# Optimization experiments

Measured on AMD Instinct MI355X. Metric: run time of the kernel, lower is better.

## Reference

```python
import jax, jax.numpy as jnp
import numpy as np

B, S, L = 32, 50, 16            # batch, seq_len, lectures per step
C, D = 50, 64                   # num_concepts, hidden_dim (key=value=summary dim)
NQ, NL, NU = 10000, 2000, 5000  # num_items, num_nonassessed_items, num_users
QV = NQ + NL + 1                # q_embed vocab (questions + lectures + pad)
QAV = 2 * NQ + 1                # qa_embed vocab
H4 = 4 * D                      # linear_dim = 4 * value_dim
EPS = 1e-5                      # torch LayerNorm default eps


def setup_inputs() -> dict:
    ks = jax.random.split(jax.random.key(0), 16)
    rn = lambda k, sh, sc: jax.random.normal(k, sh, jnp.float32) * sc
    return dict(
        q_data=jax.random.randint(ks[0], (B, S), 0, QV),
        qa_data=jax.random.randint(ks[1], (B, S), 0, QAV),
        l_data=jax.random.randint(ks[2], (B, S, L), 0, QV),
        users=jax.random.randint(ks[3], (B,), 0, NU + 1),
        key_matrix=rn(ks[4], (C, D), (2.0 / D) ** 0.5),   # key_matrix_embed rows 1..C (kaiming)
        q_embed=rn(ks[5], (QV, D), 0.02),
        qa_embed=rn(ks[6], (QAV, D), 0.02),
        u_embed=rn(ks[7], (NU + 1, D), 0.02),             # looked up but unused by write()
        M0=rn(ks[8], (C, D), (2.0 / D) ** 0.5),           # kaiming-init value matrix
        W_e=rn(ks[9], (D, D), D ** -0.5), b_e=jnp.zeros((D,), jnp.float32),
        W_a=rn(ks[10], (D, D), D ** -0.5), b_a=jnp.zeros((D,), jnp.float32),
        ln_gamma=jnp.ones((H4,), jnp.float32), ln_beta=jnp.zeros((H4,), jnp.float32),
        W0=rn(ks[11], (H4, H4), H4 ** -0.5), b0=jnp.zeros((H4,), jnp.float32),
        W1=rn(ks[12], (H4, H4), H4 ** -0.5), b1=jnp.zeros((H4,), jnp.float32),
        W_out=rn(ks[13], (H4, 1), H4 ** -0.5), b_out=jnp.zeros((1,), jnp.float32),
    )


def _forward(q_data, qa_data, l_data, key_matrix, q_embed, qa_embed, M0,
             W_e, b_e, W_a, b_a, ln_gamma, ln_beta, W0, b0, W1, b1, W_out, b_out):
    Bv = q_data.shape[0]
    q_e = q_embed[q_data]        # (B,S,D)
    qa_e = qa_embed[qa_data]     # (B,S,D)
    l_e = q_embed[l_data]        # (B,S,L,D) lectures share the q embedding table

    corr = lambda x: jax.nn.softmax(x @ key_matrix.T, axis=-1)  # softmax addressing
    q_cw = corr(q_e)             # (B,S,C)
    l_cw = corr(l_e)             # (B,S,L,C)
    # erase / add gates are memory-independent -> precompute (batched GEMMs)
    l_er = jax.nn.sigmoid(l_e @ W_e + b_e); l_ad = jnp.tanh(l_e @ W_a + b_a)
    q_er = jax.nn.sigmoid(qa_e @ W_e + b_e); q_ad = jnp.tanh(qa_e @ W_a + b_a)

    tm2 = lambda x: jnp.swapaxes(x, 0, 1)           # (B,S,..) -> (S,B,..)
    tm3 = lambda x: jnp.transpose(x, (1, 2, 0, 3))  # (B,S,L,..) -> (S,L,B,..)
    xs = (tm2(q_cw), tm2(q_e), tm2(q_er), tm2(q_ad),
          tm3(l_cw), tm3(l_e), tm3(l_er), tm3(l_ad))

    def write(M, w, e, a):  # erase-add gated write
        w = w[:, :, None]   # (B,C,1)
        return M * (1.0 - w * e[:, None, :]) + w * a[:, None, :]

    def layer_norm(x):
        mu = jnp.mean(x, -1, keepdims=True)
        v = jnp.var(x, -1, keepdims=True)
        return (x - mu) * jax.lax.rsqrt(v + EPS) * ln_gamma + ln_beta

    def outer(M, step):
        qcw, q, qer, qad, lcw, le, ler, lad = step
        q_read = jnp.einsum('bc,bcd->bd', qcw, M)  # read BEFORE lecture writes

        def inner(carry, lx):
            Mc, acc = carry
            w, e, a = lx
            acc = acc + jnp.einsum('bc,bcd->bd', w, Mc)  # read then write
            return (write(Mc, w, e, a), acc), None

        (M, l_read), _ = jax.lax.scan(inner, (M, jnp.zeros_like(q)), (lcw, ler, lad))
        # `l` after the loop is the LAST lecture embedding of this step
        mastery = layer_norm(jnp.concatenate([q_read, q, l_read, le[-1]], axis=-1))
        h = jax.nn.relu(mastery @ W0 + b0) @ W1 + b1   # dropout = identity (eval)
        pred = jax.nn.sigmoid(h @ W_out + b_out)[:, 0]
        M = write(M, qcw, qer, qad)                    # commit the q/a interaction
        return M, pred

    M_init = jnp.broadcast_to(M0, (Bv,) + M0.shape)
    _, preds = jax.lax.scan(outer, M_init, xs)
    return jnp.swapaxes(preds, 0, 1)                   # (B,S)


def reference(q_data, qa_data, l_data, users, key_matrix, q_embed, qa_embed,
              u_embed, M0, W_e, b_e, W_a, b_a, ln_gamma, ln_beta,
              W0, b0, W1, b1, W_out, b_out):
    # users/u_embed are looked up by the torch module but unused by write()'s math
    return _forward(q_data, qa_data, l_data, key_matrix, q_embed, qa_embed, M0,
                    W_e, b_e, W_a, b_a, ln_gamma, ln_beta, W0, b0, W1, b1, W_out, b_out)
```

## Files before the change

### kernel.cpp

```cpp
#include <hip/hip_runtime.h>
#include <math.h>

#define BB 32
#define SS 50
#define LL 16
#define CC 50
#define DD 64
#define NCH 13
#define H4 256
#define NROWS_Q (BB*SS)
#define NROWS_L (BB*SS*LL)

#define EA_ST 2304
#define W_ST  68

#define RB 64
#define NBLK_L (NROWS_L/RB)
#define NBLK_Q (NROWS_Q/RB)
#define NGB (NBLK_L + 2*NBLK_Q)

#define KBAT 16
#define NBAT (H4/KBAT)

static_assert(EA_ST == 17*128 + 128, "ea record: 17 slots x 64 lanes x float2, +pad");
static_assert(W_ST == 17*4, "w record: 17 slots x 4 chunk-cols");
static_assert(SS % 2 == 0, "phaseA double-step pipeline needs even SS");
static_assert(NROWS_L % RB == 0 && NROWS_Q % RB == 0, "GEMM row blocking");
static_assert(NBAT*KBAT == H4 && NBAT % 2 == 0,
              "phaseB k-loop must cover ALL of H4 in pairs of batches");

#define OFF_EA     ((size_t)0)
#define OFF_W      (OFF_EA + (size_t)NROWS_Q*EA_ST)
#define OFF_PQ     (OFF_W  + (size_t)BB*NCH*SS*W_ST)
#define OFF_PL     (OFF_PQ + (size_t)NROWS_Q*DD)
#define OFF_QE     (OFF_PL + (size_t)NROWS_Q*DD)
#define OFF_LELAST (OFF_QE + (size_t)NROWS_Q*DD)

__global__ __launch_bounds__(256) void k0_kernel(
    const int* __restrict__ qd, const int* __restrict__ qadx,
    const int* __restrict__ ld,
    const float* __restrict__ Kmat, const float* __restrict__ qemb,
    const float* __restrict__ qaemb,
    const float* __restrict__ We, const float* __restrict__ Wa,
    const float* __restrict__ be, const float* __restrict__ ba,
    float* __restrict__ eaW, float* __restrict__ wrecW,
    float* __restrict__ Pzero,
    float* __restrict__ q_e_o, float* __restrict__ le_last)
{
    __shared__ float smem[16384];
    float* sX   = smem;
    float* sW   = smem + 4096;
    float* sOut = smem + 4096;

    int tid = threadIdx.x;
    int bid = blockIdx.x;

    for (int i = bid*256 + tid; i < 2*NROWS_Q*DD; i += NGB*256) Pzero[i] = 0.f;

    int bt, base;
    if (bid < NBLK_L)              { bt = 0; base = bid*RB; }
    else if (bid < NBLK_L+NBLK_Q)  { bt = 1; base = (bid-NBLK_L)*RB; }
    else                           { bt = 2; base = (bid-NBLK_L-NBLK_Q)*RB; }

    {
        const int*   idsrc = (bt==0) ? ld : (bt==1) ? qd : qadx;
        const float* tab   = (bt==2) ? qaemb : qemb;
        for (int idx = tid; idx < RB*16; idx += 256) {
            int r = idx >> 4, q = idx & 15;
            int id = idsrc[base + r];
            *(float4*)(sX + r*64 + q*4) =
                *(const float4*)(tab + (size_t)id*DD + q*4);
        }
    }
    for (int i = tid; i < 12288; i += 256) {
        int k4 = i / 768, rem = i - k4*768;
        int c = rem >> 2, j = rem & 3;
        int k = k4*4 + j;
        float v;
        if      (c < 64)  v = We[k*64 + c];
        else if (c < 128) v = Wa[k*64 + (c-64)];
        else if (c < 178) v = Kmat[(c-128)*64 + k];
        else              v = 0.f;
        sW[i] = v;
    }
    __syncthreads();

    int rg = tid >> 5, cg = tid & 31;
    int r0 = rg*8, c0 = cg*6;
    float acc[8][6];
    #pragma unroll
    for (int i = 0; i < 8; ++i)
        #pragma unroll
        for (int c = 0; c < 6; ++c) acc[i][c] = 0.f;

    #pragma unroll 2
    for (int k4 = 0; k4 < 16; ++k4) {
        float4 xv[8], wv[6];
        #pragma unroll
        for (int i = 0; i < 8; ++i)
            xv[i] = *(const float4*)(sX + (r0+i)*64 + k4*4);
        #pragma unroll
        for (int c = 0; c < 6; ++c)
            wv[c] = *(const float4*)(sW + k4*768 + (c0+c)*4);
        #pragma unroll
        for (int i = 0; i < 8; ++i)
            #pragma unroll
            for (int c = 0; c < 6; ++c) {
                acc[i][c] = fmaf(xv[i].x, wv[c].x, acc[i][c]);
                acc[i][c] = fmaf(xv[i].y, wv[c].y, acc[i][c]);
                acc[i][c] = fmaf(xv[i].z, wv[c].z, acc[i][c]);
                acc[i][c] = fmaf(xv[i].w, wv[c].w, acc[i][c]);
            }
    }
    __syncthreads();
    #pragma unroll
    for (int i = 0; i < 8; ++i)
        #pragma unroll
        for (int c = 0; c < 6; ++c)
            sOut[(r0+i)*192 + c0 + c] = acc[i][c];
    __syncthreads();

    int lane = tid & 63, wvi = tid >> 6;
    float bev = be[lane], bav = ba[lane];

    auto rowsoftmax = [&](const float* orow) -> float {
        float sc = orow[128 + lane];
        float s = (lane < CC) ? sc : -1e30f;
        float mx = s;
        #pragma unroll
        for (int o = 32; o >= 1; o >>= 1) mx = fmaxf(mx, __shfl_xor(mx, o));
        float p = (lane < CC) ? expf(s - mx) : 0.f;
        float sum = p;
        #pragma unroll
        for (int o = 32; o >= 1; o >>= 1) sum += __shfl_xor(sum, o);
        return p / sum;
    };

    for (int i = 0; i < 16; ++i) {
        int rr = wvi*16 + i;
        int grow = base + rr;
        const float* orow = sOut + rr*192;

        if (bt == 0) {
            float erv = 1.f / (1.f + expf(-(orow[lane] + bev)));
            float adv = tanhf(orow[64 + lane] + bav);
            float wsm = rowsoftmax(orow);
            int bs = grow >> 4, il = grow & 15;
            *(float2*)(eaW + (size_t)bs*EA_ST + il*128 + lane*2) =
                make_float2(erv, adv);
            int b = bs / SS, s2 = bs - b*SS;
            if (lane < 52) {
                int omx = lane >> 2, j = lane & 3;
                wrecW[(((size_t)(b*NCH + omx)*SS + s2)*17 + il)*4 + j] =
                    (lane < CC) ? wsm : 0.f;
            }
            if (il == LL-1) le_last[(size_t)bs*DD + lane] = sX[rr*64 + lane];
        } else if (bt == 1) {
            float wsm = rowsoftmax(orow);
            int qrow = grow;
            int b = qrow / SS, s2 = qrow - b*SS;
            if (lane < 52) {
                int omx = lane >> 2, j = lane & 3;
                wrecW[(((size_t)(b*NCH + omx)*SS + s2)*17 + 16)*4 + j] =
                    (lane < CC) ? wsm : 0.f;
            }
            q_e_o[(size_t)qrow*DD + lane] = sX[rr*64 + lane];
        } else {
            float erv = 1.f / (1.f + expf(-(orow[lane] + bev)));
            float adv = tanhf(orow[64 + lane] + bav);
            int qrow = grow;
            *(float2*)(eaW + (size_t)qrow*EA_ST + 2048 + lane*2) =
                make_float2(erv, adv);
        }
    }
}

__global__ __launch_bounds__(64) void phaseA_kernel(
    const float* __restrict__ M0,
    const float* __restrict__ ea, const float* __restrict__ wrec,
    float* __restrict__ Pq, float* __restrict__ Pl)
{
    int om   = blockIdx.x >> 5;
    int b    = blockIdx.x & 31;
    int lane = threadIdx.x;
    int c0   = om * 4;

    __shared__ __align__(16) float wbuf[2][W_ST];

    float M[4];
    #pragma unroll
    for (int i = 0; i < 4; ++i) {
        int c = c0 + i;
        M[i] = (c < CC) ? M0[c*DD + lane] : 0.f;
    }

    const float* eb = ea   + (size_t)b*SS*EA_ST + lane*2;
    const float* wb = wrec + (size_t)(b*NCH + om)*SS*W_ST;
    float* pq = Pq + (size_t)b*SS*DD + lane;
    float* pl = Pl + (size_t)b*SS*DD + lane;

    float2 ea0[17], ea1[17];

    #pragma unroll
    for (int il = 0; il < 17; ++il)
        ea0[il] = *(const float2*)(eb + il*128);
    if (lane < 17)
        *(float4*)&wbuf[0][lane*4] = *(const float4*)(wb + lane*4);

    auto step = [&](int s, float2 (&cur)[17], float2 (&nxt)[17], int wbsel) {
        bool pf = (s < SS-1);
        float4 rw;
        if (pf) {
            const float* eg = eb + (size_t)(s+1)*EA_ST;
            #pragma unroll
            for (int il = 0; il < 17; ++il)
                nxt[il] = *(const float2*)(eg + il*128);
            if (lane < 17)
                rw = *(const float4*)(wb + (size_t)(s+1)*W_ST + lane*4);
        }

        float4 qw = *(const float4*)&wbuf[wbsel][64];
        float qr;
        qr = qw.x * M[0];
        qr = fmaf(qw.y, M[1], qr);
        qr = fmaf(qw.z, M[2], qr);
        qr = fmaf(qw.w, M[3], qr);

        float a0 = 0.f, a1 = 0.f, a2 = 0.f, a3 = 0.f;
        #pragma unroll
        for (int il = 0; il < 16; ++il) {
            float4 w = *(const float4*)&wbuf[wbsel][il*4];
            float e = cur[il].x, a = cur[il].y;
            a0 = fmaf(w.x, M[0], a0);
            a1 = fmaf(w.y, M[1], a1);
            a2 = fmaf(w.z, M[2], a2);
            a3 = fmaf(w.w, M[3], a3);
            M[0] = fmaf(w.x, fmaf(-e, M[0], a), M[0]);
            M[1] = fmaf(w.y, fmaf(-e, M[1], a), M[1]);
            M[2] = fmaf(w.z, fmaf(-e, M[2], a), M[2]);
            M[3] = fmaf(w.w, fmaf(-e, M[3], a), M[3]);
        }

        atomicAdd(pq + (size_t)s*DD, qr);
        atomicAdd(pl + (size_t)s*DD, (a0 + a1) + (a2 + a3));

        {
            float e = cur[16].x, a = cur[16].y;
            M[0] = fmaf(qw.x, fmaf(-e, M[0], a), M[0]);
            M[1] = fmaf(qw.y, fmaf(-e, M[1], a), M[1]);
            M[2] = fmaf(qw.z, fmaf(-e, M[2], a), M[2]);
            M[3] = fmaf(qw.w, fmaf(-e, M[3], a), M[3]);
        }

        if (pf && lane < 17)
            *(float4*)&wbuf[wbsel ^ 1][lane*4] = rw;
    };

    for (int s = 0; s < SS; s += 2) {
        step(s,     ea0, ea1, 0);
        step(s + 1, ea1, ea0, 1);
    }
}

__global__ __launch_bounds__(256) void phaseB_kernel(
    const float* __restrict__ Pq, const float* __restrict__ Pl,
    const float* __restrict__ q_e_i, const float* __restrict__ le_last,
    const float* __restrict__ ln_g, const float* __restrict__ ln_b,
    const float* __restrict__ W0, const float* __restrict__ b0,
    const float* __restrict__ W1, const float* __restrict__ b1,
    const float* __restrict__ Wout, const float* __restrict__ bout,
    float* __restrict__ out)
{
    __shared__ float m[8][H4];
    __shared__ float h[8][H4];
    __shared__ float red[8][4];

    int j = threadIdx.x;
    int g0 = blockIdx.x * 8;
    int lane = j & 63, wv = j >> 6;

    int seg = j >> 6, dd = j & 63;
    #pragma unroll
    for (int r = 0; r < 8; ++r) {
        int g = g0 + r;
        float v;
        if      (seg == 0) v = Pq[(size_t)g*DD + dd];
        else if (seg == 1) v = q_e_i[(size_t)g*DD + dd];
        else if (seg == 2) v = Pl[(size_t)g*DD + dd];
        else               v = le_last[(size_t)g*DD + dd];
        m[r][j] = v;
    }
    __syncthreads();

    #pragma unroll
    for (int rr = 0; rr < 2; ++rr) {
        int r = wv + rr*4;
        float4 v4 = *(((const float4*)&m[r][0]) + lane);
        float s1 = v4.x + v4.y + v4.z + v4.w;
        float s2 = v4.x*v4.x + v4.y*v4.y + v4.z*v4.z + v4.w*v4.w;
        #pragma unroll
        for (int o = 32; o >= 1; o >>= 1) {
            s1 += __shfl_xor(s1, o);
            s2 += __shfl_xor(s2, o);
        }
        float mu  = s1 * (1.f/256.f);
        float var = s2 * (1.f/256.f) - mu*mu;
        float is  = rsqrtf(var + 1e-5f);
        float4 g4 = *(((const float4*)ln_g) + lane);
        float4 b4 = *(((const float4*)ln_b) + lane);
        float4 o4;
        o4.x = (v4.x - mu)*is*g4.x + b4.x;
        o4.y = (v4.y - mu)*is*g4.y + b4.y;
        o4.z = (v4.z - mu)*is*g4.z + b4.z;
        o4.w = (v4.w - mu)*is*g4.w + b4.w;
        *(((float4*)&m[r][0]) + lane) = o4;
    }
    __syncthreads();

    const float* Wp = W0 + j;
    float acc[8];
    {
        float bj = b0[j];
        #pragma unroll
        for (int r = 0; r < 8; ++r) acc[r] = bj;
    }
    {
        float wA[KBAT], wB[KBAT];
        #pragma unroll
        for (int t = 0; t < KBAT; ++t) wA[t] = Wp[(size_t)t*H4];
        #pragma unroll 1
        for (int kb = 0; kb < NBAT; kb += 2) {
            #pragma unroll
            for (int t = 0; t < KBAT; ++t)
                wB[t] = Wp[(size_t)((kb+1)*KBAT + t)*H4];
            #pragma unroll
            for (int t4 = 0; t4 < KBAT/4; ++t4) {
                #pragma unroll
                for (int r = 0; r < 8; ++r) {
                    float4 mv = *(const float4*)&m[r][kb*KBAT + t4*4];
                    acc[r] = fmaf(mv.x, wA[t4*4+0], acc[r]);
                    acc[r] = fmaf(mv.y, wA[t4*4+1], acc[r]);
                    acc[r] = fmaf(mv.z, wA[t4*4+2], acc[r]);
                    acc[r] = fmaf(mv.w, wA[t4*4+3], acc[r]);
                }
            }
            if (kb + 2 < NBAT) {
                #pragma unroll
                for (int t = 0; t < KBAT; ++t)
                    wA[t] = Wp[(size_t)((kb+2)*KBAT + t)*H4];
            }
            #pragma unroll
            for (int t4 = 0; t4 < KBAT/4; ++t4) {
                #pragma unroll
                for (int r = 0; r < 8; ++r) {
                    float4 mv = *(const float4*)&m[r][(kb+1)*KBAT + t4*4];
                    acc[r] = fmaf(mv.x, wB[t4*4+0], acc[r]);
                    acc[r] = fmaf(mv.y, wB[t4*4+1], acc[r]);
                    acc[r] = fmaf(mv.z, wB[t4*4+2], acc[r]);
                    acc[r] = fmaf(mv.w, wB[t4*4+3], acc[r]);
                }
            }
        }
    }
    #pragma unroll
    for (int r = 0; r < 8; ++r) h[r][j] = fmaxf(acc[r], 0.f);
    __syncthreads();

    const float* Wp1 = W1 + j;
    float a2[8];
    {
        float bj = b1[j];
        #pragma unroll
        for (int r = 0; r < 8; ++r) a2[r] = bj;
    }
    {
        float wA[KBAT], wB[KBAT];
        #pragma unroll
        for (int t = 0; t < KBAT; ++t) wA[t] = Wp1[(size_t)t*H4];
        #pragma unroll 1
        for (int kb = 0; kb < NBAT; kb += 2) {
            #pragma unroll
            for (int t = 0; t < KBAT; ++t)
                wB[t] = Wp1[(size_t)((kb+1)*KBAT + t)*H4];
            #pragma unroll
            for (int t4 = 0; t4 < KBAT/4; ++t4) {
                #pragma unroll
                for (int r = 0; r < 8; ++r) {
                    float4 hv = *(const float4*)&h[r][kb*KBAT + t4*4];
                    a2[r] = fmaf(hv.x, wA[t4*4+0], a2[r]);
                    a2[r] = fmaf(hv.y, wA[t4*4+1], a2[r]);
                    a2[r] = fmaf(hv.z, wA[t4*4+2], a2[r]);
                    a2[r] = fmaf(hv.w, wA[t4*4+3], a2[r]);
                }
            }
            if (kb + 2 < NBAT) {
                #pragma unroll
                for (int t = 0; t < KBAT; ++t)
                    wA[t] = Wp1[(size_t)((kb+2)*KBAT + t)*H4];
            }
            #pragma unroll
            for (int t4 = 0; t4 < KBAT/4; ++t4) {
                #pragma unroll
                for (int r = 0; r < 8; ++r) {
                    float4 hv = *(const float4*)&h[r][(kb+1)*KBAT + t4*4];
                    a2[r] = fmaf(hv.x, wB[t4*4+0], a2[r]);
                    a2[r] = fmaf(hv.y, wB[t4*4+1], a2[r]);
                    a2[r] = fmaf(hv.z, wB[t4*4+2], a2[r]);
                    a2[r] = fmaf(hv.w, wB[t4*4+3], a2[r]);
                }
            }
        }
    }

    float wo = Wout[j];
    #pragma unroll
    for (int r = 0; r < 8; ++r) {
        float v = a2[r] * wo;
        #pragma unroll
        for (int o = 32; o >= 1; o >>= 1) v += __shfl_xor(v, o);
        if (lane == 0) red[r][wv] = v;
    }
    __syncthreads();
    if (j < 8) {
        float t = red[j][0] + red[j][1] + red[j][2] + red[j][3] + bout[0];
        out[g0 + j] = 1.f / (1.f + expf(-t));
    }
}

extern "C" void kernel_launch(void* const* d_in, const int* in_sizes, int n_in,
                              void* d_out, int out_size, void* d_ws, size_t ws_size,
                              hipStream_t stream)
{
    const int*   q_data  = (const int*)  d_in[0];
    const int*   qa_data = (const int*)  d_in[1];
    const int*   l_data  = (const int*)  d_in[2];
    const float* Kmat    = (const float*)d_in[4];
    const float* q_embed = (const float*)d_in[5];
    const float* qa_embed= (const float*)d_in[6];
    const float* M0      = (const float*)d_in[8];
    const float* W_e     = (const float*)d_in[9];
    const float* b_e     = (const float*)d_in[10];
    const float* W_a     = (const float*)d_in[11];
    const float* b_a     = (const float*)d_in[12];
    const float* ln_g    = (const float*)d_in[13];
    const float* ln_b    = (const float*)d_in[14];
    const float* W0      = (const float*)d_in[15];
    const float* b0      = (const float*)d_in[16];
    const float* W1      = (const float*)d_in[17];
    const float* b1      = (const float*)d_in[18];
    const float* W_out   = (const float*)d_in[19];
    const float* b_out   = (const float*)d_in[20];

    float* ws = (float*)d_ws;
    float* eaW     = ws + OFF_EA;
    float* wrecW   = ws + OFF_W;
    float* Pq      = ws + OFF_PQ;
    float* Pl      = ws + OFF_PL;
    float* q_e     = ws + OFF_QE;
    float* le_last = ws + OFF_LELAST;

    float* out = (float*)d_out;

    k0_kernel<<<NGB, 256, 0, stream>>>(q_data, qa_data, l_data,
                                       Kmat, q_embed, qa_embed,
                                       W_e, W_a, b_e, b_a,
                                       eaW, wrecW, Pq,
                                       q_e, le_last);
    phaseA_kernel<<<BB*NCH, 64, 0, stream>>>(M0, eaW, wrecW, Pq, Pl);
    phaseB_kernel<<<NROWS_Q/8, 256, 0, stream>>>(Pq, Pl, q_e, le_last,
                                                 ln_g, ln_b, W0, b0, W1, b1,
                                                 W_out, b_out, out);
}
```

Baseline: 211.8 us.

## Restructure k0 GEMM to per-lane column accumulators with halved shared memory

The projection GEMM in k0 now gives each lane one output column per gate (erase, add, softmax score) and 16 rows per wave, so results stay in registers. This removes the shared-memory output staging pass and its extra barrier. The weight tile is loaded in two k-halves, which cuts shared memory from 64KB to about 40KB, and launch bounds now request 4 blocks per SM to raise occupancy. In exchange there is an extra stage-and-sync step, the weight loads are per-lane scalars, the X float4 loads are broadcast across lanes, and the kernel needs 48 accumulators per thread.

```diff
diff --git a/kernel.cpp b/kernel.cpp
--- a/kernel.cpp
+++ b/kernel.cpp
@@ -36,7 +36,7 @@
 #define OFF_QE     (OFF_PL + (size_t)NROWS_Q*DD)
 #define OFF_LELAST (OFF_QE + (size_t)NROWS_Q*DD)
 
-__global__ __launch_bounds__(256) void k0_kernel(
+__global__ __launch_bounds__(256, 4) void k0_kernel(
     const int* __restrict__ qd, const int* __restrict__ qadx,
     const int* __restrict__ ld,
     const float* __restrict__ Kmat, const float* __restrict__ qemb,
@@ -47,10 +47,8 @@
     float* __restrict__ Pzero,
     float* __restrict__ q_e_o, float* __restrict__ le_last)
 {
-    __shared__ float smem[16384];
-    float* sX   = smem;
-    float* sW   = smem + 4096;
-    float* sOut = smem + 4096;
+    __shared__ float sX[RB*DD];
+    __shared__ float sW[32*192];
 
     int tid = threadIdx.x;
     int bid = blockIdx.x;
@@ -72,60 +70,104 @@
                 *(const float4*)(tab + (size_t)id*DD + q*4);
         }
     }
-    for (int i = tid; i < 12288; i += 256) {
-        int k4 = i / 768, rem = i - k4*768;
-        int c = rem >> 2, j = rem & 3;
-        int k = k4*4 + j;
-        float v;
-        if      (c < 64)  v = We[k*64 + c];
-        else if (c < 128) v = Wa[k*64 + (c-64)];
-        else if (c < 178) v = Kmat[(c-128)*64 + k];
-        else              v = 0.f;
-        sW[i] = v;
-    }
-    __syncthreads();
-
-    int rg = tid >> 5, cg = tid & 31;
-    int r0 = rg*8, c0 = cg*6;
-    float acc[8][6];
-    #pragma unroll
-    for (int i = 0; i < 8; ++i)
-        #pragma unroll
-        for (int c = 0; c < 6; ++c) acc[i][c] = 0.f;
+
+    auto stageW = [&](int kb) {
+        #pragma unroll
+        for (int n = 0; n < 4; ++n) {
+            int f  = n*256 + tid;
+            int kl = f >> 5, cf = f & 31;
+            int k  = kb + kl;
+            const float* src = (cf < 16) ? (We + k*64 + cf*4)
+                                         : (Wa + k*64 + (cf-16)*4);
+            *(float4*)(sW + kl*192 + cf*4) = *(const float4*)src;
+        }
+        #pragma unroll
+        for (int n = 0; n < 8; ++n) {
+            int f  = n*256 + tid;
+            int kl = f >> 6, cr = f & 63;
+            int k  = kb + kl;
+            sW[kl*192 + 128 + cr] = (cr < CC) ? Kmat[cr*64 + k] : 0.f;
+        }
+    };
+
+    int lane = tid & 63, wvi = tid >> 6;
+    int r0 = wvi * 16;
+
+    float accE[16], accA[16], accS[16];
+    #pragma unroll
+    for (int r = 0; r < 16; ++r) { accE[r] = 0.f; accA[r] = 0.f; accS[r] = 0.f; }
+
+    stageW(0);
+    __syncthreads();
 
     #pragma unroll 2
-    for (int k4 = 0; k4 < 16; ++k4) {
-        float4 xv[8], wv[6];
-        #pragma unroll
-        for (int i = 0; i < 8; ++i)
-            xv[i] = *(const float4*)(sX + (r0+i)*64 + k4*4);
-        #pragma unroll
-        for (int c = 0; c < 6; ++c)
-            wv[c] = *(const float4*)(sW + k4*768 + (c0+c)*4);
-        #pragma unroll
-        for (int i = 0; i < 8; ++i)
-            #pragma unroll
-            for (int c = 0; c < 6; ++c) {
-                acc[i][c] = fmaf(xv[i].x, wv[c].x, acc[i][c]);
-                acc[i][c] = fmaf(xv[i].y, wv[c].y, acc[i][c]);
-                acc[i][c] = fmaf(xv[i].z, wv[c].z, acc[i][c]);
-                acc[i][c] = fmaf(xv[i].w, wv[c].w, acc[i][c]);
-            }
-    }
-    __syncthreads();
-    #pragma unroll
-    for (int i = 0; i < 8; ++i)
-        #pragma unroll
-        for (int c = 0; c < 6; ++c)
-            sOut[(r0+i)*192 + c0 + c] = acc[i][c];
-    __syncthreads();
-
-    int lane = tid & 63, wvi = tid >> 6;
+    for (int k4 = 0; k4 < 8; ++k4) {
+        float wE[4], wA4[4], wS[4];
+        #pragma unroll
+        for (int kk = 0; kk < 4; ++kk) {
+            int krow = (k4*4 + kk)*192;
+            wE[kk]  = sW[krow + lane];
+            wA4[kk] = sW[krow + 64 + lane];
+            wS[kk]  = sW[krow + 128 + lane];
+        }
+        #pragma unroll
+        for (int r = 0; r < 16; ++r) {
+            float4 xv = *(const float4*)(sX + (r0+r)*64 + k4*4);
+            accE[r] = fmaf(xv.x, wE[0], accE[r]);
+            accE[r] = fmaf(xv.y, wE[1], accE[r]);
+            accE[r] = fmaf(xv.z, wE[2], accE[r]);
+            accE[r] = fmaf(xv.w, wE[3], accE[r]);
+            accA[r] = fmaf(xv.x, wA4[0], accA[r]);
+            accA[r] = fmaf(xv.y, wA4[1], accA[r]);
+            accA[r] = fmaf(xv.z, wA4[2], accA[r]);
+            accA[r] = fmaf(xv.w, wA4[3], accA[r]);
+            accS[r] = fmaf(xv.x, wS[0], accS[r]);
+            accS[r] = fmaf(xv.y, wS[1], accS[r]);
+            accS[r] = fmaf(xv.z, wS[2], accS[r]);
+            accS[r] = fmaf(xv.w, wS[3], accS[r]);
+        }
+    }
+    __syncthreads();
+
+    stageW(32);
+    __syncthreads();
+
+    #pragma unroll 2
+    for (int k4 = 0; k4 < 8; ++k4) {
+        float wE[4], wA4[4], wS[4];
+        #pragma unroll
+        for (int kk = 0; kk < 4; ++kk) {
+            int krow = (k4*4 + kk)*192;
+            wE[kk]  = sW[krow + lane];
+            wA4[kk] = sW[krow + 64 + lane];
+            wS[kk]  = sW[krow + 128 + lane];
+        }
+        #pragma unroll
+        for (int r = 0; r < 16; ++r) {
+            float4 xv = *(const float4*)(sX + (r0+r)*64 + 32 + k4*4);
+            accE[r] = fmaf(xv.x, wE[0], accE[r]);
+            accE[r] = fmaf(xv.y, wE[1], accE[r]);
+            accE[r] = fmaf(xv.z, wE[2], accE[r]);
+            accE[r] = fmaf(xv.w, wE[3], accE[r]);
+            accA[r] = fmaf(xv.x, wA4[0], accA[r]);
+            accA[r] = fmaf(xv.y, wA4[1], accA[r]);
+            accA[r] = fmaf(xv.z, wA4[2], accA[r]);
+            accA[r] = fmaf(xv.w, wA4[3], accA[r]);
+            accS[r] = fmaf(xv.x, wS[0], accS[r]);
+            accS[r] = fmaf(xv.y, wS[1], accS[r]);
+            accS[r] = fmaf(xv.z, wS[2], accS[r]);
+            accS[r] = fmaf(xv.w, wS[3], accS[r]);
+        }
+    }
+
     float bev = be[lane], bav = ba[lane];
 
-    auto rowsoftmax = [&](const float* orow) -> float {
-        float sc = orow[128 + lane];
-        float s = (lane < CC) ? sc : -1e30f;
+    #pragma unroll
+    for (int r = 0; r < 16; ++r) {
+        int rr = r0 + r;
+        int grow = base + rr;
+
+        float s = (lane < CC) ? accS[r] : -1e30f;
         float mx = s;
         #pragma unroll
         for (int o = 32; o >= 1; o >>= 1) mx = fmaxf(mx, __shfl_xor(mx, o));
@@ -133,18 +175,11 @@
         float sum = p;
         #pragma unroll
         for (int o = 32; o >= 1; o >>= 1) sum += __shfl_xor(sum, o);
-        return p / sum;
-    };
-
-    for (int i = 0; i < 16; ++i) {
-        int rr = wvi*16 + i;
-        int grow = base + rr;
-        const float* orow = sOut + rr*192;
+        float wsm = p / sum;
 
         if (bt == 0) {
-            float erv = 1.f / (1.f + expf(-(orow[lane] + bev)));
-            float adv = tanhf(orow[64 + lane] + bav);
-            float wsm = rowsoftmax(orow);
+            float erv = 1.f / (1.f + expf(-(accE[r] + bev)));
+            float adv = tanhf(accA[r] + bav);
             int bs = grow >> 4, il = grow & 15;
             *(float2*)(eaW + (size_t)bs*EA_ST + il*128 + lane*2) =
                 make_float2(erv, adv);
@@ -156,7 +191,6 @@
             }
             if (il == LL-1) le_last[(size_t)bs*DD + lane] = sX[rr*64 + lane];
         } else if (bt == 1) {
-            float wsm = rowsoftmax(orow);
             int qrow = grow;
             int b = qrow / SS, s2 = qrow - b*SS;
             if (lane < 52) {
@@ -166,8 +200,8 @@
             }
             q_e_o[(size_t)qrow*DD + lane] = sX[rr*64 + lane];
         } else {
-            float erv = 1.f / (1.f + expf(-(orow[lane] + bev)));
-            float adv = tanhf(orow[64 + lane] + bav);
+            float erv = 1.f / (1.f + expf(-(accE[r] + bev)));
+            float adv = tanhf(accA[r] + bav);
             int qrow = grow;
             *(float2*)(eaW + (size_t)qrow*EA_ST + 2048 + lane*2) =
                 make_float2(erv, adv);
```

Result: faster. 206.6 us (-2.5%).
